# Kernel optimization log

Measured on AMD Instinct MI355X. Metric: run time of the kernel, lower is better.

Reference implementation:

```python
import jax, jax.numpy as jnp
import numpy as np
from functools import partial

D = 1024
H = 4 * D
E = 8
K_TOP = 2
B, T = 4, 2048
NEG_INF = jnp.float32(-1e30)


def setup_inputs() -> dict:
    key = jax.random.key(0)
    ks = jax.random.split(key, 12)
    s = 0.02
    return {
        "x": jax.random.normal(ks[0], (B, T, D), jnp.float32),
        "noise": jax.random.normal(ks[1], (B, T, E), jnp.float32),
        "gate_w": jax.random.normal(ks[2], (E, D), jnp.float32) * s,
        "gate_b": jnp.zeros((E,), jnp.float32),
        "var_w": jax.random.normal(ks[3], (E, D), jnp.float32) * s,
        "var_b": jnp.zeros((E,), jnp.float32),
        "w1": jax.random.normal(ks[4], (E, H, D), jnp.float32) * s,
        "b1": jnp.zeros((E, H), jnp.float32),
        "w2": jax.random.normal(ks[5], (E, D, H), jnp.float32) * s,
        "b2": jnp.zeros((E, D), jnp.float32),
    }


def reference(x, noise, gate_w, gate_b, var_w, var_b, w1, b1, w2, b2):
    # Noisy top-k gating
    logits = jnp.einsum("btd,ed->bte", x, gate_w) + gate_b          # [B,T,E]
    std = jax.nn.softplus(jnp.einsum("btd,ed->bte", x, var_w) + var_b)
    noisy = logits + noise * std                                      # [B,T,E]
    _, idx = jax.lax.top_k(noisy, K_TOP)                              # [B,T,K]
    # boolean top-k mask over experts
    mask = (idx[..., None] == jnp.arange(E)).any(axis=-2)             # [B,T,E]
    coef = jax.nn.softmax(jnp.where(mask, noisy, NEG_INF), axis=-1)   # zeros outside top-k

    # Combine: sum_e coef_e * FFN_e(x). coef is exactly 0 for non-selected
    # experts, so this equals the masked gather/scatter math. Scan over the
    # small expert dim to avoid a [E,B,T,H] intermediate.
    coef_e = jnp.moveaxis(coef, -1, 0)                                # [E,B,T]

    def body(acc, ew):
        w1e, b1e, w2e, b2e, ce = ew
        h = jax.nn.relu(jnp.einsum("btd,hd->bth", x, w1e) + b1e)
        y = jnp.einsum("bth,dh->btd", h, w2e) + b2e
        return acc + y * ce[..., None], None

    out, _ = jax.lax.scan(body, jnp.zeros_like(x), (w1, b1, w2, b2, coef_e))
    return out
```

## Files before the change

kernel.cpp:

```cpp
#include <hip/hip_runtime.h>
#include <hip/hip_bf16.h>
#include <math.h>

#define NTOK 8192
#define DD   1024
#define HH   4096
#define NE   8
#define BM 256
#define BN 256
#define BK 64
#define SLOT_CAP (2 * NTOK + NE * BM)

typedef __bf16 bf16;
typedef __bf16 bf16x8 __attribute__((ext_vector_type(8)));
typedef __bf16 bf16x4 __attribute__((ext_vector_type(4)));
typedef float  f32x4  __attribute__((ext_vector_type(4)));

typedef __attribute__((address_space(3))) unsigned char lds_u8;
typedef const __attribute__((address_space(1))) unsigned char g_u8;

__device__ __forceinline__ void gload16(const bf16* g, bf16* l) {
  __builtin_amdgcn_global_load_lds((g_u8*)g, (lds_u8*)l, 16, 0, 0);
}

__device__ __forceinline__ float softplus_f(float v) {
  return fmaxf(v, 0.f) + log1pf(expf(-fabsf(v)));
}

__global__ __launch_bounds__(64) void moe_gate_kernel(
    const float* __restrict__ x, const float* __restrict__ noise,
    const float* __restrict__ gate_w, const float* __restrict__ gate_b,
    const float* __restrict__ var_w,  const float* __restrict__ var_b,
    float* __restrict__ coef2, int* __restrict__ t2e, int* __restrict__ counts)
{
  const int t = blockIdx.x;
  const int lane = threadIdx.x;
  const float* xt = x + (size_t)t * DD;
  float pg[NE], pv[NE];
  #pragma unroll
  for (int e = 0; e < NE; ++e) { pg[e] = 0.f; pv[e] = 0.f; }
  #pragma unroll 4
  for (int i = 0; i < DD / 64; ++i) {
    const int d = lane + i * 64;
    const float xv = xt[d];
    #pragma unroll
    for (int e = 0; e < NE; ++e) {
      pg[e] = fmaf(xv, gate_w[e * DD + d], pg[e]);
      pv[e] = fmaf(xv, var_w[e * DD + d], pv[e]);
    }
  }
  #pragma unroll
  for (int e = 0; e < NE; ++e) {
    #pragma unroll
    for (int off = 32; off; off >>= 1) {
      pg[e] += __shfl_xor(pg[e], off);
      pv[e] += __shfl_xor(pv[e], off);
    }
  }
  if (lane == 0) {
    float noisy[NE];
    #pragma unroll
    for (int e = 0; e < NE; ++e) {
      const float lg = pg[e] + gate_b[e];
      const float sd = softplus_f(pv[e] + var_b[e]);
      noisy[e] = lg + noise[t * NE + e] * sd;
    }
    int i1 = 0; float n1 = noisy[0];
    #pragma unroll
    for (int e = 1; e < NE; ++e) if (noisy[e] > n1) { n1 = noisy[e]; i1 = e; }
    int i2 = -1; float n2 = -3.0e38f;
    #pragma unroll
    for (int e = 0; e < NE; ++e) if (e != i1 && noisy[e] > n2) { n2 = noisy[e]; i2 = e; }
    const float e2 = expf(n2 - n1);
    const float den = 1.f + e2;
    coef2[t * 2 + 0] = 1.f / den;
    coef2[t * 2 + 1] = e2 / den;
    t2e[t * 2 + 0] = i1;
    t2e[t * 2 + 1] = i2;
    atomicAdd(&counts[i1], 1);
    atomicAdd(&counts[i2], 1);
  }
}

__global__ void moe_offsets_kernel(const int* __restrict__ counts, int* __restrict__ po) {
  if (threadIdx.x == 0) {
    int acc = 0;
    po[0] = 0;
    for (int e = 0; e < NE; ++e) {
      acc += ((counts[e] + BM - 1) / BM) * BM;
      po[e + 1] = acc;
    }
  }
}

__global__ __launch_bounds__(256) void moe_scatter_kernel(
    const int* __restrict__ t2e, const float* __restrict__ coef2,
    const int* __restrict__ po, int* __restrict__ cnt2,
    int* __restrict__ assign_tok, float* __restrict__ slot_coef)
{
  const int t = blockIdx.x * 256 + threadIdx.x;
  if (t >= NTOK) return;
  #pragma unroll
  for (int k = 0; k < 2; ++k) {
    const int e = t2e[t * 2 + k];
    const int pos = atomicAdd(&cnt2[e], 1);
    const int slot = po[e] + pos;
    assign_tok[slot] = t;
    slot_coef[slot] = coef2[t * 2 + k];
  }
}

__global__ __launch_bounds__(256) void cvt_bf16_kernel(const float* __restrict__ src,
                                                       bf16* __restrict__ dst, int n4) {
  for (int i = blockIdx.x * 256 + threadIdx.x; i < n4; i += gridDim.x * 256) {
    const float4 f = ((const float4*)src)[i];
    bf16x4 v;
    v[0] = (bf16)f.x; v[1] = (bf16)f.y; v[2] = (bf16)f.z; v[3] = (bf16)f.w;
    ((bf16x4*)dst)[i] = v;
  }
}

template<int KDIM, int NCOLS, bool FFN1>
__global__ __launch_bounds__(512, 2) void moe_gemm_kernel(
    const bf16* __restrict__ Asrc, const bf16* __restrict__ Wsrc,
    const float* __restrict__ bias,
    const int* __restrict__ assign_tok, const float* __restrict__ slot_coef,
    const int* __restrict__ po,
    bf16* __restrict__ hout, float* __restrict__ out,
    int chunk_base, int gx)
{
  __shared__ bf16 smA[2][BM * BK];
  __shared__ bf16 smB[2][BN * BK];
  __shared__ int toks[BM];

  const int nwg = gx * (NCOLS / BN);
  const int lin = blockIdx.x;
  const int q = nwg >> 3, r = nwg & 7;
  const int xcd = lin & 7, idx = lin >> 3;
  const int wg = (xcd < r ? xcd * (q + 1) : r * (q + 1) + (xcd - r) * q) + idx;
  const int bx = wg % gx, by = wg / gx;

  const int row0 = chunk_base + bx * BM;
  const int po8 = po[NE];
  if (row0 >= po8) return;
  int e = 0;
  while (row0 >= po[e + 1]) ++e;
  const int bn0 = by * BN;
  const bf16* We = Wsrc + (size_t)e * ((size_t)HH * DD);

  const int tid = threadIdx.x, lane = tid & 63;
  if (tid < BM) toks[tid] = assign_tok[row0 + tid];
  __syncthreads();

  const int t7 = tid & 7;
  const bf16* aptr[4];
  const bf16* bptr[4];
  #pragma unroll
  for (int i = 0; i < 4; ++i) {
    const int g = i * 512 + tid;
    const int row = g >> 3;
    const int c8 = ((t7 ^ (row & 7)) * 8);
    int ar;
    if constexpr (FFN1) {
      const int s = toks[row];
      ar = s < 0 ? 0 : s;
    } else {
      ar = row0 - chunk_base + row;
    }
    aptr[i] = Asrc + (size_t)ar * KDIM + c8;
    bptr[i] = We + (size_t)(bn0 + row) * KDIM + c8;
  }

  auto stage = [&](int sel, int k0) {
    #pragma unroll
    for (int i = 0; i < 4; ++i)
      gload16(aptr[i] + k0, &smA[sel][(i * 512 + tid) * 8]);
    #pragma unroll
    for (int i = 0; i < 4; ++i)
      gload16(bptr[i] + k0, &smB[sel][(i * 512 + tid) * 8]);
  };

  const int wid = tid >> 6, wr = wid >> 2, wc = wid & 3;
  const int la = lane & 15, hi = lane >> 4;
  f32x4 acc[8][4];
  #pragma unroll
  for (int m = 0; m < 8; ++m)
    #pragma unroll
    for (int n = 0; n < 4; ++n) acc[m][n] = {0.f, 0.f, 0.f, 0.f};

  constexpr int NK = KDIM / BK;
  stage(0, 0);
  __syncthreads();
  #pragma unroll 2
  for (int ks = 0; ks < NK; ++ks) {
    const int cur = ks & 1;
    if (ks + 1 < NK) stage(cur ^ 1, (ks + 1) * BK);
    const bf16* A = smA[cur];
    const bf16* B = smB[cur];
    #pragma unroll
    for (int kk = 0; kk < 2; ++kk) {
      bf16x8 af[8], bf_[4];
      #pragma unroll
      for (int m = 0; m < 8; ++m) {
        const int rw = wr * 128 + m * 16 + la;
        const int c8 = ((kk * 4 + hi) ^ (rw & 7)) * 8;
        af[m] = *(const bf16x8*)(A + rw * 64 + c8);
      }
      #pragma unroll
      for (int n = 0; n < 4; ++n) {
        const int rw = wc * 64 + n * 16 + la;
        const int c8 = ((kk * 4 + hi) ^ (rw & 7)) * 8;
        bf_[n] = *(const bf16x8*)(B + rw * 64 + c8);
      }
      #pragma unroll
      for (int m = 0; m < 8; ++m)
        #pragma unroll
        for (int n = 0; n < 4; ++n)
          acc[m][n] = __builtin_amdgcn_mfma_f32_16x16x32_bf16(af[m], bf_[n], acc[m][n], 0, 0, 0);
    }
    __syncthreads();
  }

  if constexpr (FFN1) {
    #pragma unroll
    for (int n = 0; n < 4; ++n) {
      const int col = bn0 + wc * 64 + n * 16 + la;
      const float bb = bias[e * NCOLS + col];
      #pragma unroll
      for (int m = 0; m < 8; ++m) {
        const int rl = wr * 128 + m * 16 + hi * 4;
        #pragma unroll
        for (int rr = 0; rr < 4; ++rr) {
          float v = acc[m][n][rr] + bb;
          v = v > 0.f ? v : 0.f;
          hout[(size_t)(row0 - chunk_base + rl + rr) * HH + col] = (bf16)v;
        }
      }
    }
  } else {
    #pragma unroll
    for (int n = 0; n < 4; ++n) {
      const int col = bn0 + wc * 64 + n * 16 + la;
      const float bb = bias[e * NCOLS + col];
      #pragma unroll
      for (int m = 0; m < 8; ++m) {
        const int rl = wr * 128 + m * 16 + hi * 4;
        #pragma unroll
        for (int rr = 0; rr < 4; ++rr) {
          const int tl = rl + rr;
          const int tok = toks[tl];
          if (tok >= 0) {
            const float c = slot_coef[row0 + tl];
            atomicAdd(out + (size_t)tok * DD + col, c * (acc[m][n][rr] + bb));
          }
        }
      }
    }
  }
}

extern "C" void kernel_launch(void* const* d_in, const int* in_sizes, int n_in,
                              void* d_out, int out_size, void* d_ws, size_t ws_size,
                              hipStream_t stream) {
  const float* x      = (const float*)d_in[0];
  const float* noise  = (const float*)d_in[1];
  const float* gate_w = (const float*)d_in[2];
  const float* gate_b = (const float*)d_in[3];
  const float* var_w  = (const float*)d_in[4];
  const float* var_b  = (const float*)d_in[5];
  const float* w1     = (const float*)d_in[6];
  const float* b1     = (const float*)d_in[7];
  const float* w2     = (const float*)d_in[8];
  const float* b2     = (const float*)d_in[9];
  float* out = (float*)d_out;
  (void)in_sizes; (void)n_in; (void)out_size;

  char* ws = (char*)d_ws;
  size_t off = 0;
  auto alloc = [&](size_t bytes) {
    off = (off + 255) & ~(size_t)255;
    size_t o = off;
    off += bytes;
    return o;
  };
  bf16*  xb         = (bf16*)(ws + alloc((size_t)NTOK * DD * 2));
  float* coef2      = (float*)(ws + alloc((size_t)NTOK * 2 * 4));
  int*   t2e        = (int*)(ws + alloc((size_t)NTOK * 2 * 4));
  int*   counts     = (int*)(ws + alloc(64));
  int*   cnt2       = counts + 8;
  int*   po         = (int*)(ws + alloc(64));
  int*   assign_tok = (int*)(ws + alloc((size_t)SLOT_CAP * 4));
  float* slot_coef  = (float*)(ws + alloc((size_t)SLOT_CAP * 4));
  bf16*  w1b        = (bf16*)(ws + alloc((size_t)NE * HH * DD * 2));
  bf16*  w2b        = (bf16*)(ws + alloc((size_t)NE * DD * HH * 2));
  off = (off + 255) & ~(size_t)255;
  const size_t h_avail = ws_size > off ? ws_size - off : 0;
  int chunk_rows = (int)(h_avail / ((size_t)HH * 2));
  chunk_rows = (chunk_rows / BM) * BM;
  if (chunk_rows < BM) chunk_rows = BM;
  if (chunk_rows > SLOT_CAP) chunk_rows = SLOT_CAP;
  bf16* hbuf = (bf16*)(ws + off);

  hipMemsetAsync(counts, 0, 64, stream);
  hipMemsetAsync(assign_tok, 0xFF, (size_t)SLOT_CAP * 4, stream);
  hipMemsetAsync(out, 0, (size_t)NTOK * DD * 4, stream);

  moe_gate_kernel<<<NTOK, 64, 0, stream>>>(x, noise, gate_w, gate_b, var_w, var_b,
                                           coef2, t2e, counts);
  moe_offsets_kernel<<<1, 64, 0, stream>>>(counts, po);
  moe_scatter_kernel<<<NTOK / 256, 256, 0, stream>>>(t2e, coef2, po, cnt2,
                                                     assign_tok, slot_coef);
  cvt_bf16_kernel<<<2048, 256, 0, stream>>>(x, xb, NTOK * DD / 4);
  cvt_bf16_kernel<<<2048, 256, 0, stream>>>(w1, w1b, NE * HH * DD / 4);
  cvt_bf16_kernel<<<2048, 256, 0, stream>>>(w2, w2b, NE * DD * HH / 4);

  const int rounds = (SLOT_CAP + chunk_rows - 1) / chunk_rows;
  for (int r = 0; r < rounds; ++r) {
    const int cb = r * chunk_rows;
    const int rows_here = (cb + chunk_rows <= SLOT_CAP) ? chunk_rows : (SLOT_CAP - cb);
    const int gx = rows_here / BM;
    moe_gemm_kernel<DD, HH, true><<<gx * (HH / BN), 512, 0, stream>>>(
        xb, w1b, b1, assign_tok, slot_coef, po, hbuf, nullptr, cb, gx);
    moe_gemm_kernel<HH, DD, false><<<gx * (DD / BN), 512, 0, stream>>>(
        hbuf, w2b, b2, assign_tok, slot_coef, po, nullptr, out, cb, gx);
  }
}
```

Baseline: 995.0 us.

## Shrink GEMM tiles to 128x128, drop double buffering, fuse x conversion into gate

The expert GEMMs move from 256x256 tiles with 512 threads and double-buffered LDS to 128x128 tiles with 256 threads and a single LDS buffer. Each k-step now loads, syncs and computes. FFN2 gets a different block index mapping that walks columns first. The fp32-to-bf16 conversion of x is folded into the gating kernel, which removes one launch and one extra read of x. Smaller tiles give more blocks and less padding, but they cost more weight traffic, and without double buffering the load latency is no longer overlapped with the MFMA work.

```diff
diff --git a/kernel.cpp b/kernel.cpp
--- a/kernel.cpp
+++ b/kernel.cpp
@@ -6,8 +6,8 @@
 #define DD   1024
 #define HH   4096
 #define NE   8
-#define BM 256
-#define BN 256
+#define BM 128
+#define BN 128
 #define BK 64
 #define SLOT_CAP (2 * NTOK + NE * BM)
 
@@ -31,11 +31,13 @@
     const float* __restrict__ x, const float* __restrict__ noise,
     const float* __restrict__ gate_w, const float* __restrict__ gate_b,
     const float* __restrict__ var_w,  const float* __restrict__ var_b,
-    float* __restrict__ coef2, int* __restrict__ t2e, int* __restrict__ counts)
+    float* __restrict__ coef2, int* __restrict__ t2e, int* __restrict__ counts,
+    bf16* __restrict__ xb)
 {
   const int t = blockIdx.x;
   const int lane = threadIdx.x;
   const float* xt = x + (size_t)t * DD;
+  bf16* xbt = xb + (size_t)t * DD;
   float pg[NE], pv[NE];
   #pragma unroll
   for (int e = 0; e < NE; ++e) { pg[e] = 0.f; pv[e] = 0.f; }
@@ -43,6 +45,7 @@
   for (int i = 0; i < DD / 64; ++i) {
     const int d = lane + i * 64;
     const float xv = xt[d];
+    xbt[d] = (bf16)xv;
     #pragma unroll
     for (int e = 0; e < NE; ++e) {
       pg[e] = fmaf(xv, gate_w[e * DD + d], pg[e]);
@@ -121,7 +124,7 @@
 }
 
 template<int KDIM, int NCOLS, bool FFN1>
-__global__ __launch_bounds__(512, 2) void moe_gemm_kernel(
+__global__ __launch_bounds__(256) void moe_gemm_kernel(
     const bf16* __restrict__ Asrc, const bf16* __restrict__ Wsrc,
     const float* __restrict__ bias,
     const int* __restrict__ assign_tok, const float* __restrict__ slot_coef,
@@ -129,37 +132,38 @@
     bf16* __restrict__ hout, float* __restrict__ out,
     int chunk_base, int gx)
 {
-  __shared__ bf16 smA[2][BM * BK];
-  __shared__ bf16 smB[2][BN * BK];
+  __shared__ bf16 As[BM][BK];
+  __shared__ bf16 Bs[BN][BK];
   __shared__ int toks[BM];
 
-  const int nwg = gx * (NCOLS / BN);
+  const int nwg = gridDim.x;
   const int lin = blockIdx.x;
   const int q = nwg >> 3, r = nwg & 7;
   const int xcd = lin & 7, idx = lin >> 3;
   const int wg = (xcd < r ? xcd * (q + 1) : r * (q + 1) + (xcd - r) * q) + idx;
-  const int bx = wg % gx, by = wg / gx;
-
+  int bx, by;
+  if constexpr (FFN1) { bx = wg % gx; by = wg / gx; }
+  else               { by = wg % (NCOLS / BN); bx = wg / (NCOLS / BN); }
+
+  const int po8 = po[NE];
   const int row0 = chunk_base + bx * BM;
-  const int po8 = po[NE];
   if (row0 >= po8) return;
   int e = 0;
   while (row0 >= po[e + 1]) ++e;
   const int bn0 = by * BN;
   const bf16* We = Wsrc + (size_t)e * ((size_t)HH * DD);
-
-  const int tid = threadIdx.x, lane = tid & 63;
+  const int tid = threadIdx.x, lane = tid & 63, wave = tid >> 6;
   if (tid < BM) toks[tid] = assign_tok[row0 + tid];
   __syncthreads();
 
-  const int t7 = tid & 7;
-  const bf16* aptr[4];
-  const bf16* bptr[4];
+  const int rin = lane >> 3;
+  const int c8s = ((lane & 7) ^ rin) * 8;
+  const bf16* asrc[4];
+  const bf16* bsrc[4];
   #pragma unroll
   for (int i = 0; i < 4; ++i) {
-    const int g = i * 512 + tid;
-    const int row = g >> 3;
-    const int c8 = ((t7 ^ (row & 7)) * 8);
+    const int c = wave * 4 + i;
+    const int row = c * 8 + rin;
     int ar;
     if constexpr (FFN1) {
       const int s = toks[row];
@@ -167,90 +171,79 @@
     } else {
       ar = row0 - chunk_base + row;
     }
-    aptr[i] = Asrc + (size_t)ar * KDIM + c8;
-    bptr[i] = We + (size_t)(bn0 + row) * KDIM + c8;
-  }
-
-  auto stage = [&](int sel, int k0) {
-    #pragma unroll
-    for (int i = 0; i < 4; ++i)
-      gload16(aptr[i] + k0, &smA[sel][(i * 512 + tid) * 8]);
-    #pragma unroll
-    for (int i = 0; i < 4; ++i)
-      gload16(bptr[i] + k0, &smB[sel][(i * 512 + tid) * 8]);
-  };
-
-  const int wid = tid >> 6, wr = wid >> 2, wc = wid & 3;
+    asrc[i] = Asrc + (size_t)ar * KDIM + c8s;
+    bsrc[i] = We + (size_t)(bn0 + row) * KDIM + c8s;
+  }
+
   const int la = lane & 15, hi = lane >> 4;
-  f32x4 acc[8][4];
-  #pragma unroll
-  for (int m = 0; m < 8; ++m)
+  const int wm = (wave >> 1) * 64, wn = (wave & 1) * 64;
+  f32x4 acc[4][4];
+  #pragma unroll
+  for (int m = 0; m < 4; ++m)
     #pragma unroll
     for (int n = 0; n < 4; ++n) acc[m][n] = {0.f, 0.f, 0.f, 0.f};
 
-  constexpr int NK = KDIM / BK;
-  stage(0, 0);
-  __syncthreads();
-  #pragma unroll 2
-  for (int ks = 0; ks < NK; ++ks) {
-    const int cur = ks & 1;
-    if (ks + 1 < NK) stage(cur ^ 1, (ks + 1) * BK);
-    const bf16* A = smA[cur];
-    const bf16* B = smB[cur];
-    #pragma unroll
-    for (int kk = 0; kk < 2; ++kk) {
-      bf16x8 af[8], bf_[4];
-      #pragma unroll
-      for (int m = 0; m < 8; ++m) {
-        const int rw = wr * 128 + m * 16 + la;
-        const int c8 = ((kk * 4 + hi) ^ (rw & 7)) * 8;
-        af[m] = *(const bf16x8*)(A + rw * 64 + c8);
+  for (int k0 = 0; k0 < KDIM; k0 += BK) {
+    #pragma unroll
+    for (int i = 0; i < 4; ++i) gload16(asrc[i] + k0, &As[(wave * 4 + i) * 8][0]);
+    #pragma unroll
+    for (int i = 0; i < 4; ++i) gload16(bsrc[i] + k0, &Bs[(wave * 4 + i) * 8][0]);
+    __syncthreads();
+    #pragma unroll
+    for (int ks = 0; ks < 2; ++ks) {
+      bf16x8 af[4], bff[4];
+      #pragma unroll
+      for (int m = 0; m < 4; ++m) {
+        const int row = wm + m * 16 + la;
+        const int c8 = (ks * 4 + hi) ^ (row & 7);
+        af[m] = *(const bf16x8*)(&As[row][c8 * 8]);
       }
       #pragma unroll
       for (int n = 0; n < 4; ++n) {
-        const int rw = wc * 64 + n * 16 + la;
-        const int c8 = ((kk * 4 + hi) ^ (rw & 7)) * 8;
-        bf_[n] = *(const bf16x8*)(B + rw * 64 + c8);
+        const int row = wn + n * 16 + la;
+        const int c8 = (ks * 4 + hi) ^ (row & 7);
+        bff[n] = *(const bf16x8*)(&Bs[row][c8 * 8]);
       }
       #pragma unroll
-      for (int m = 0; m < 8; ++m)
+      for (int m = 0; m < 4; ++m)
         #pragma unroll
         for (int n = 0; n < 4; ++n)
-          acc[m][n] = __builtin_amdgcn_mfma_f32_16x16x32_bf16(af[m], bf_[n], acc[m][n], 0, 0, 0);
+          acc[m][n] = __builtin_amdgcn_mfma_f32_16x16x32_bf16(af[m], bff[n], acc[m][n], 0, 0, 0);
     }
     __syncthreads();
   }
 
   if constexpr (FFN1) {
+    const int hrow0 = row0 - chunk_base;
     #pragma unroll
     for (int n = 0; n < 4; ++n) {
-      const int col = bn0 + wc * 64 + n * 16 + la;
+      const int col = bn0 + wn + n * 16 + la;
       const float bb = bias[e * NCOLS + col];
       #pragma unroll
-      for (int m = 0; m < 8; ++m) {
-        const int rl = wr * 128 + m * 16 + hi * 4;
+      for (int m = 0; m < 4; ++m) {
+        const int rbase = wm + m * 16 + hi * 4;
         #pragma unroll
         for (int rr = 0; rr < 4; ++rr) {
           float v = acc[m][n][rr] + bb;
           v = v > 0.f ? v : 0.f;
-          hout[(size_t)(row0 - chunk_base + rl + rr) * HH + col] = (bf16)v;
+          hout[(size_t)(hrow0 + rbase + rr) * HH + col] = (bf16)v;
         }
       }
     }
   } else {
     #pragma unroll
     for (int n = 0; n < 4; ++n) {
-      const int col = bn0 + wc * 64 + n * 16 + la;
+      const int col = bn0 + wn + n * 16 + la;
       const float bb = bias[e * NCOLS + col];
       #pragma unroll
-      for (int m = 0; m < 8; ++m) {
-        const int rl = wr * 128 + m * 16 + hi * 4;
+      for (int m = 0; m < 4; ++m) {
+        const int rbase = wm + m * 16 + hi * 4;
         #pragma unroll
         for (int rr = 0; rr < 4; ++rr) {
-          const int tl = rl + rr;
-          const int tok = toks[tl];
+          const int trow = rbase + rr;
+          const int tok = toks[trow];
           if (tok >= 0) {
-            const float c = slot_coef[row0 + tl];
+            const float c = slot_coef[row0 + trow];
             atomicAdd(out + (size_t)tok * DD + col, c * (acc[m][n][rr] + bb));
           }
         }
@@ -306,11 +299,10 @@
   hipMemsetAsync(out, 0, (size_t)NTOK * DD * 4, stream);
 
   moe_gate_kernel<<<NTOK, 64, 0, stream>>>(x, noise, gate_w, gate_b, var_w, var_b,
-                                           coef2, t2e, counts);
+                                           coef2, t2e, counts, xb);
   moe_offsets_kernel<<<1, 64, 0, stream>>>(counts, po);
   moe_scatter_kernel<<<NTOK / 256, 256, 0, stream>>>(t2e, coef2, po, cnt2,
                                                      assign_tok, slot_coef);
-  cvt_bf16_kernel<<<2048, 256, 0, stream>>>(x, xb, NTOK * DD / 4);
   cvt_bf16_kernel<<<2048, 256, 0, stream>>>(w1, w1b, NE * HH * DD / 4);
   cvt_bf16_kernel<<<2048, 256, 0, stream>>>(w2, w2b, NE * DD * HH / 4);
 
@@ -319,9 +311,9 @@
     const int cb = r * chunk_rows;
     const int rows_here = (cb + chunk_rows <= SLOT_CAP) ? chunk_rows : (SLOT_CAP - cb);
     const int gx = rows_here / BM;
-    moe_gemm_kernel<DD, HH, true><<<gx * (HH / BN), 512, 0, stream>>>(
+    moe_gemm_kernel<DD, HH, true><<<gx * (HH / BN), 256, 0, stream>>>(
         xb, w1b, b1, assign_tok, slot_coef, po, hbuf, nullptr, cb, gx);
-    moe_gemm_kernel<HH, DD, false><<<gx * (DD / BN), 512, 0, stream>>>(
+    moe_gemm_kernel<HH, DD, false><<<gx * (DD / BN), 256, 0, stream>>>(
         hbuf, w2b, b2, assign_tok, slot_coef, po, nullptr, out, cb, gx);
   }
 }
```

Measured after the change: 956.6 us. -3.9%, faster.
